# Kernel tuning notes

Hardware: AMD Instinct MI355X
Metric: run time of the kernel (lower is better)

## Reference

```python
import jax, jax.numpy as jnp
import numpy as np

N_NODES = 100000
N_EDGES = 1600000
IN_DIM, HID, OUT_DIM = 512, 32, 40


def setup_inputs() -> dict:
    key = jax.random.key(0)
    ks = jax.random.split(key, 6)
    x = jax.random.normal(ks[0], (N_NODES, IN_DIM), dtype=jnp.float32)
    edge_index = jax.random.randint(ks[1], (2, N_EDGES), 0, N_NODES, dtype=jnp.int64)
    # Glorot-ish init for the linear weights
    W1 = jax.random.normal(ks[2], (IN_DIM, HID), dtype=jnp.float32) / np.sqrt(IN_DIM)
    b1 = jnp.zeros((HID,), dtype=jnp.float32)
    W2 = jax.random.normal(ks[3], (HID, OUT_DIM), dtype=jnp.float32) / np.sqrt(HID)
    b2 = jnp.zeros((OUT_DIM,), dtype=jnp.float32)
    return {"x": x, "edge_index": edge_index, "W1": W1, "b1": b1, "W2": W2, "b2": b2}


def gcn_conv(x, W, b, src, dst, n_nodes):
    """PyG GCNConv: h = D^{-1/2} (A + I) D^{-1/2} (x W) + b."""
    h = x @ W  # linear transform first (reduces edge-level traffic)
    # add self-loops
    loop = jnp.arange(n_nodes, dtype=src.dtype)
    s = jnp.concatenate([src, loop])
    d = jnp.concatenate([dst, loop])
    # symmetric normalization from in-degree (including self-loops)
    deg = jax.ops.segment_sum(jnp.ones_like(d, dtype=h.dtype), d, num_segments=n_nodes)
    dinv = jnp.where(deg > 0, jax.lax.rsqrt(deg), 0.0)
    norm = dinv[s] * dinv[d]  # [E+N]
    msg = h[s] * norm[:, None]  # gather + scale
    out = jax.ops.segment_sum(msg, d, num_segments=n_nodes)  # scatter-add
    return out + b


def reference(x, edge_index, W1, b1, W2, b2):
    src, dst = edge_index[0], edge_index[1]
    n = x.shape[0]
    h = jax.nn.relu(gcn_conv(x, W1, b1, src, dst, n))
    # dropout is identity in eval mode (reference runs in eval)
    out = gcn_conv(h, W2, b2, src, dst, n)
    return out
```

## Files before the change

kernel.cpp:

```cpp
#include <hip/hip_runtime.h>
#include <hip/hip_bf16.h>

#define N_IN 512
#define HID 32
#define OUTD 40
#define NCOPY 8

typedef __attribute__((ext_vector_type(8))) short bf16x8;
typedef __attribute__((ext_vector_type(4))) float f32x4;


__global__ void k_init(int* __restrict__ csr, int tot4, int* __restrict__ cnt8,
                       int n8_4, int n, float* __restrict__ g1, float* __restrict__ p)
{
    int i = blockIdx.x * blockDim.x + threadIdx.x;
    if (i < tot4) {
        int4 v = make_int4(n, n, n, n);
        *(int4*)&csr[(size_t)i * 4] = v;
    }
    if (i < n8_4) {
        int4 z4 = make_int4(0, 0, 0, 0);
        *(int4*)&cnt8[(size_t)i * 4] = z4;
    }
    if (blockIdx.x == 0) {
        float4 z = make_float4(0.f, 0.f, 0.f, 0.f);
        if (threadIdx.x < 8)
            *(float4*)&g1[(size_t)n * HID + threadIdx.x * 4] = z;
        else if (threadIdx.x < 16)
            *(float4*)&p[(size_t)n * HID + (threadIdx.x - 8) * 4] = z;
    }
}

__global__ void k_count(const int* __restrict__ dst, int* __restrict__ cnt8,
                        int* __restrict__ rankp, int n, int e)
{
    int c = blockIdx.x & (NCOPY - 1);
    int* mycnt = cnt8 + (size_t)c * n;
    int i = (blockIdx.x * blockDim.x + threadIdx.x) * 4;
    if (i + 3 < e) {
        int4 d4 = *(const int4*)&dst[i];
        int r0 = atomicAdd(&mycnt[d4.x], 1);
        int r1 = atomicAdd(&mycnt[d4.y], 1);
        int r2 = atomicAdd(&mycnt[d4.z], 1);
        int r3 = atomicAdd(&mycnt[d4.w], 1);
        int hc = c << 24;
        *(int4*)&rankp[i] = make_int4(hc | r0, hc | r1, hc | r2, hc | r3);
    } else if (i < e) {
        for (int k = i; k < e; k++) {
            int r = atomicAdd(&mycnt[dst[k]], 1);
            rankp[k] = (c << 24) | r;
        }
    }
}

__global__ void k_bases(int* __restrict__ cnt8, int* __restrict__ cnt, int n)
{
    int d = blockIdx.x * blockDim.x + threadIdx.x;
    if (d >= n) return;
    int s = 0;
#pragma unroll
    for (int c = 0; c < NCOPY; c++) {
        int v = cnt8[(size_t)c * n + d];
        cnt8[(size_t)c * n + d] = s;
        s += v;
    }
    cnt[d] = s;
}

__global__ __launch_bounds__(256) void k_scan1(const int* __restrict__ cnt,
                                               int* __restrict__ offs,
                                               int* __restrict__ bsums, int n)
{
    __shared__ int sm[256];
    int t = threadIdx.x;
    int base = blockIdx.x * 1024 + t * 4;
    int a0 = (base + 0 < n) ? cnt[base + 0] : 0;
    int a1 = (base + 1 < n) ? cnt[base + 1] : 0;
    int a2 = (base + 2 < n) ? cnt[base + 2] : 0;
    int a3 = (base + 3 < n) ? cnt[base + 3] : 0;
    int d0 = (a0 + 15) & ~15;
    int d1 = (a1 + 15) & ~15;
    int d2 = (a2 + 15) & ~15;
    int d3 = (a3 + 15) & ~15;
    int s = d0 + d1 + d2 + d3;
    sm[t] = s;
    __syncthreads();
#pragma unroll
    for (int off = 1; off < 256; off <<= 1) {
        int v = (t >= off) ? sm[t - off] : 0;
        __syncthreads();
        sm[t] += v;
        __syncthreads();
    }
    int excl = sm[t] - s;
    if (base + 0 < n) offs[base + 0] = excl;
    if (base + 1 < n) offs[base + 1] = excl + d0;
    if (base + 2 < n) offs[base + 2] = excl + d0 + d1;
    if (base + 3 < n) offs[base + 3] = excl + d0 + d1 + d2;
    if (t == 255) bsums[blockIdx.x] = sm[255];
}

__global__ __launch_bounds__(256) void k_scan2(int* bsums, int nb)
{
    __shared__ int sm[256];
    int t = threadIdx.x;
    int s = (t < nb) ? bsums[t] : 0;
    sm[t] = s;
    __syncthreads();
#pragma unroll
    for (int off = 1; off < 256; off <<= 1) {
        int v = (t >= off) ? sm[t - off] : 0;
        __syncthreads();
        sm[t] += v;
        __syncthreads();
    }
    if (t < nb) bsums[t] = sm[t] - s;
}

__global__ void k_scan3(int* __restrict__ offs, const int* __restrict__ bsums,
                        const int* __restrict__ cnt, float* __restrict__ dinv, int n)
{
    int i = blockIdx.x * blockDim.x + threadIdx.x;
    if (i >= n) return;
    offs[i] = offs[i] + bsums[i >> 10];
    dinv[i] = rsqrtf((float)(cnt[i] + 1));
}

__global__ void k_pos(const int* __restrict__ dst, const int* __restrict__ offs,
                      const int* __restrict__ cnt8, int* __restrict__ rankp,
                      int n, int e)
{
    int i = (blockIdx.x * blockDim.x + threadIdx.x) * 4;
    if (i >= e) return;
    if (i + 3 < e) {
        int4 d4 = *(const int4*)&dst[i];
        int4 rp = *(const int4*)&rankp[i];
        int dd[4] = {d4.x, d4.y, d4.z, d4.w};
        int rr[4] = {rp.x, rp.y, rp.z, rp.w};
        int pp[4];
#pragma unroll
        for (int k = 0; k < 4; k++) {
            int d = dd[k];
            int c = ((unsigned)rr[k]) >> 24;
            int r = rr[k] & 0xFFFFFF;
            pp[k] = offs[d] + cnt8[(size_t)c * n + d] + r;
        }
        *(int4*)&rankp[i] = make_int4(pp[0], pp[1], pp[2], pp[3]);
    } else {
        for (int k = i; k < e; k++) {
            int d = dst[k];
            int r = rankp[k];
            int c = ((unsigned)r) >> 24;
            r &= 0xFFFFFF;
            rankp[k] = offs[d] + cnt8[(size_t)c * n + d] + r;
        }
    }
}

__global__ void k_fill(const int* __restrict__ src, const int* __restrict__ pos,
                       int* __restrict__ csr, int e)
{
    int i = (blockIdx.x * blockDim.x + threadIdx.x) * 4;
    if (i >= e) return;
    if (i + 3 < e) {
        int4 p4 = *(const int4*)&pos[i];
        int4 s4 = *(const int4*)&src[i];
        csr[p4.x] = s4.x;
        csr[p4.y] = s4.y;
        csr[p4.z] = s4.z;
        csr[p4.w] = s4.w;
    } else {
        for (int k = i; k < e; k++) csr[pos[k]] = src[k];
    }
}

__global__ void k_convw(const float* __restrict__ W, unsigned short* __restrict__ wfh,
                        unsigned short* __restrict__ wfl)
{
    int idx = blockIdx.x * blockDim.x + threadIdx.x;
    int j     = idx & 7;
    int lane  = (idx >> 3) & 63;
    int ntile = (idx >> 9) & 1;
    int kstep = idx >> 10;
    int k    = kstep * 32 + (lane >> 4) * 8 + j;
    int ncol = ntile * 16 + (lane & 15);
    float v = W[k * HID + ncol];
    unsigned u = __builtin_bit_cast(unsigned, v);
    unsigned short h = (unsigned short)(u >> 16);
    float hv = __builtin_bit_cast(float, u & 0xFFFF0000u);
    float rem = v - hv;
    unsigned ur = __builtin_bit_cast(unsigned, rem);
    ur += 0x7FFF + ((ur >> 16) & 1);
    wfh[idx] = h;
    wfl[idx] = (unsigned short)(ur >> 16);
}

__global__ __launch_bounds__(256) void k_gemm1(
    const float* __restrict__ x,
    const unsigned short* __restrict__ wfh, const unsigned short* __restrict__ wfl,
    const float* __restrict__ dinv, float* __restrict__ g1, int n)
{
    const int t    = threadIdx.x;
    const int lane = t & 63;
    const int wave = t >> 6;
    const int m    = lane & 15;
    const int quad = lane >> 4;
    const int row0 = blockIdx.x * 64 + wave * 16;

    int arow = row0 + m;
    if (arow >= n) arow = n - 1;
    const float* xp = x + (size_t)arow * N_IN + quad * 8;

    f32x4 acc0 = {0.f, 0.f, 0.f, 0.f};
    f32x4 acc1 = {0.f, 0.f, 0.f, 0.f};

    for (int ks = 0; ks < 16; ks++) {
        float4 xa = *(const float4*)(xp + ks * 32);
        float4 xb = *(const float4*)(xp + ks * 32 + 4);
        float xe[8] = {xa.x, xa.y, xa.z, xa.w, xb.x, xb.y, xb.z, xb.w};
        bf16x8 ah, al;
#pragma unroll
        for (int j = 0; j < 8; j++) {
            unsigned u = __builtin_bit_cast(unsigned, xe[j]);
            ah[j] = (short)(u >> 16);
            float hv = __builtin_bit_cast(float, u & 0xFFFF0000u);
            float rem = xe[j] - hv;
            unsigned ur = __builtin_bit_cast(unsigned, rem);
            ur += 0x7FFF + ((ur >> 16) & 1);
            al[j] = (short)(ur >> 16);
        }
        bf16x8 bh0 = *(const bf16x8*)(wfh + ((size_t)(ks * 2 + 0) * 64 + lane) * 8);
        bf16x8 bh1 = *(const bf16x8*)(wfh + ((size_t)(ks * 2 + 1) * 64 + lane) * 8);
        bf16x8 bl0 = *(const bf16x8*)(wfl + ((size_t)(ks * 2 + 0) * 64 + lane) * 8);
        bf16x8 bl1 = *(const bf16x8*)(wfl + ((size_t)(ks * 2 + 1) * 64 + lane) * 8);

        acc0 = __builtin_amdgcn_mfma_f32_16x16x32_bf16(ah, bh0, acc0, 0, 0, 0);
        acc0 = __builtin_amdgcn_mfma_f32_16x16x32_bf16(al, bh0, acc0, 0, 0, 0);
        acc0 = __builtin_amdgcn_mfma_f32_16x16x32_bf16(ah, bl0, acc0, 0, 0, 0);
        acc1 = __builtin_amdgcn_mfma_f32_16x16x32_bf16(ah, bh1, acc1, 0, 0, 0);
        acc1 = __builtin_amdgcn_mfma_f32_16x16x32_bf16(al, bh1, acc1, 0, 0, 0);
        acc1 = __builtin_amdgcn_mfma_f32_16x16x32_bf16(ah, bl1, acc1, 0, 0, 0);
    }

#pragma unroll
    for (int r = 0; r < 4; r++) {
        int row = row0 + quad * 4 + r;
        if (row < n) {
            float dv = dinv[row];
            g1[(size_t)row * HID + m]      = acc0[r] * dv;
            g1[(size_t)row * HID + 16 + m] = acc1[r] * dv;
        }
    }
}


__global__ void k_agg1(const int* __restrict__ csr, const int* __restrict__ offs,
                       const int* __restrict__ cnt, const float* __restrict__ g,
                       const float* __restrict__ dinv, const float* __restrict__ b1,
                       float* __restrict__ p, int n)
{
    int gid = blockIdx.x * blockDim.x + threadIdx.x;
    int r  = gid >> 4;
    int sl = gid & 15;
    if (r >= n) return;
    int s0 = offs[r];
    int dp = (cnt[r] + 15) & ~15;
    int half = sl >> 3;
    int c = sl & 7;
    const float* gc = g + c * 4;
    float4 acc = make_float4(0.f, 0.f, 0.f, 0.f);
    if (half == 0) acc = *(const float4*)&gc[(size_t)r * HID];
    for (int b = 0; b < dp; b += 16) {
        int s = csr[s0 + b + sl];
#pragma unroll
        for (int jj = 0; jj < 8; jj++) {
            int sj = __shfl(s, jj + (half << 3), 16);
            float4 v = *(const float4*)&gc[(size_t)sj * HID];
            acc.x += v.x; acc.y += v.y; acc.z += v.z; acc.w += v.w;
        }
    }
    float4 o;
    o.x = __shfl(acc.x, sl ^ 8, 16);
    o.y = __shfl(acc.y, sl ^ 8, 16);
    o.z = __shfl(acc.z, sl ^ 8, 16);
    o.w = __shfl(acc.w, sl ^ 8, 16);
    if (half == 0) {
        float dv = dinv[r];
        float4 bv = *(const float4*)&b1[c * 4];
        float4 hp;
        hp.x = dv * fmaxf((acc.x + o.x) * dv + bv.x, 0.f);
        hp.y = dv * fmaxf((acc.y + o.y) * dv + bv.y, 0.f);
        hp.z = dv * fmaxf((acc.z + o.z) * dv + bv.z, 0.f);
        hp.w = dv * fmaxf((acc.w + o.w) * dv + bv.w, 0.f);
        *(float4*)&p[(size_t)r * HID + c * 4] = hp;
    }
}

__global__ void k_agg2_out(const int* __restrict__ csr, const int* __restrict__ offs,
                           const int* __restrict__ cnt, const float* __restrict__ g,
                           const float* __restrict__ dinv, const float* __restrict__ W2,
                           const float* __restrict__ b2, float* __restrict__ out, int n)
{
    int gid = blockIdx.x * blockDim.x + threadIdx.x;
    int r  = gid >> 4;
    int sl = gid & 15;
    if (r >= n) return;
    int s0 = offs[r];
    int dp = (cnt[r] + 15) & ~15;
    int half = sl >> 3;
    int c = sl & 7;
    const float* gc = g + c * 4;
    float4 acc = make_float4(0.f, 0.f, 0.f, 0.f);
    if (half == 0) acc = *(const float4*)&gc[(size_t)r * HID];
    for (int b = 0; b < dp; b += 16) {
        int s = csr[s0 + b + sl];
#pragma unroll
        for (int jj = 0; jj < 8; jj++) {
            int sj = __shfl(s, jj + (half << 3), 16);
            float4 v = *(const float4*)&gc[(size_t)sj * HID];
            acc.x += v.x; acc.y += v.y; acc.z += v.z; acc.w += v.w;
        }
    }
    float4 o;
    o.x = __shfl(acc.x, sl ^ 8, 16);
    o.y = __shfl(acc.y, sl ^ 8, 16);
    o.z = __shfl(acc.z, sl ^ 8, 16);
    o.w = __shfl(acc.w, sl ^ 8, 16);
    float dv = dinv[r];
    float h0 = (acc.x + o.x) * dv;
    float h1 = (acc.y + o.y) * dv;
    float h2 = (acc.z + o.z) * dv;
    float h3 = (acc.w + o.w) * dv;

    int oc = (sl < 10) ? sl * 4 : 0;
    float4 ov = *(const float4*)&b2[oc];
#pragma unroll
    for (int k4 = 0; k4 < 8; k4++) {
        float a0 = __shfl(h0, k4, 16);
        float a1 = __shfl(h1, k4, 16);
        float a2 = __shfl(h2, k4, 16);
        float a3 = __shfl(h3, k4, 16);
        float4 w0 = *(const float4*)&W2[(4 * k4 + 0) * OUTD + oc];
        float4 w1 = *(const float4*)&W2[(4 * k4 + 1) * OUTD + oc];
        float4 w2 = *(const float4*)&W2[(4 * k4 + 2) * OUTD + oc];
        float4 w3 = *(const float4*)&W2[(4 * k4 + 3) * OUTD + oc];
        ov.x += a0 * w0.x + a1 * w1.x + a2 * w2.x + a3 * w3.x;
        ov.y += a0 * w0.y + a1 * w1.y + a2 * w2.y + a3 * w3.y;
        ov.z += a0 * w0.z + a1 * w1.z + a2 * w2.z + a3 * w3.z;
        ov.w += a0 * w0.w + a1 * w1.w + a2 * w2.w + a3 * w3.w;
    }
    if (sl < 10) *(float4*)&out[(size_t)r * OUTD + sl * 4] = ov;
}

extern "C" void kernel_launch(void* const* d_in, const int* in_sizes, int n_in,
                              void* d_out, int out_size, void* d_ws, size_t ws_size,
                              hipStream_t stream)
{
    const float* x  = (const float*)d_in[0];
    const int*   ei = (const int*)d_in[1];
    const float* W1 = (const float*)d_in[2];
    const float* b1 = (const float*)d_in[3];
    const float* W2 = (const float*)d_in[4];
    const float* b2 = (const float*)d_in[5];
    float* out = (float*)d_out;

    const int n = in_sizes[0] / N_IN;
    const int e = in_sizes[1] / 2;
    const int* src = ei;
    const int* dst = ei + e;

    const int csr_cap = e + 16 * n;

    char* w = (char*)d_ws;
    float* dinv   = (float*)w;            w += sizeof(float) * (size_t)((n + 3) & ~3);
    float* g1     = (float*)w;            w += sizeof(float) * (size_t)(n + 1) * HID;
    float* p      = (float*)w;            w += sizeof(float) * (size_t)(n + 1) * HID;
    int*   cnt    = (int*)w;              w += sizeof(int) * (size_t)((n + 3) & ~3);
    int*   offs   = (int*)w;              w += sizeof(int) * (size_t)((n + 3) & ~3);
    int*   cnt8   = (int*)w;              w += sizeof(int) * (size_t)NCOPY * ((n + 3) & ~3);
    int*   rankp  = (int*)w;              w += sizeof(int) * (size_t)((e + 3) & ~3);
    int*   bsums  = (int*)w;              w += sizeof(int) * 1024;
    unsigned short* wfh = (unsigned short*)w;  w += sizeof(unsigned short) * 16384;
    unsigned short* wfl = (unsigned short*)w;  w += sizeof(unsigned short) * 16384;
    int*   csr    = (int*)w;              w += sizeof(int) * (size_t)((csr_cap + 3) & ~3);

    const int nb = (n + 1023) / 1024;
    const int ec = (e + 3) / 4;
    const int n8_4 = (NCOPY * n + 3) / 4;
    const int tot4 = (csr_cap + 3) / 4;
    const int initN = (tot4 > n8_4) ? tot4 : n8_4;

    k_init<<<(initN + 255) / 256, 256, 0, stream>>>(csr, tot4, cnt8, n8_4, n, g1, p);
    k_count<<<(ec + 255) / 256, 256, 0, stream>>>(dst, cnt8, rankp, n, e);
    k_bases<<<(n + 255) / 256, 256, 0, stream>>>(cnt8, cnt, n);
    k_scan1<<<nb, 256, 0, stream>>>(cnt, offs, bsums, n);
    k_scan2<<<1, 256, 0, stream>>>(bsums, nb);
    k_scan3<<<(n + 255) / 256, 256, 0, stream>>>(offs, bsums, cnt, dinv, n);
    k_pos<<<(ec + 255) / 256, 256, 0, stream>>>(dst, offs, cnt8, rankp, n, e);
    k_fill<<<(ec + 255) / 256, 256, 0, stream>>>(src, rankp, csr, e);

    k_convw<<<64, 256, 0, stream>>>(W1, wfh, wfl);

    k_gemm1<<<(n + 63) / 64, 256, 0, stream>>>(x, wfh, wfl, dinv, g1, n);

    int t16 = n * 16;
    k_agg1<<<(t16 + 255) / 256, 256, 0, stream>>>(csr, offs, cnt, g1, dinv, b1, p, n);
    k_agg2_out<<<(t16 + 255) / 256, 256, 0, stream>>>(csr, offs, cnt, p, dinv, W2, b2, out, n);
}
```

Before: 510.1 us.

## Store hidden features in fp16 and fuse CSR position and fill kernels

Switches the intermediate feature buffers g1 and p from fp32 to fp16, halving the bytes moved by the random row gathers in both aggregation kernels. The aggregation lanes are remapped so each lane loads eight halves per gather, with a two-step shuffle reduction. The position and fill kernels are merged so computed CSR positions are used directly instead of being written to and reread from rankp. The cost is fp16 rounding of intermediate activations, which lowers accuracy.

```diff
diff --git a/kernel.cpp b/kernel.cpp
--- a/kernel.cpp
+++ b/kernel.cpp
@@ -8,10 +8,11 @@
 
 typedef __attribute__((ext_vector_type(8))) short bf16x8;
 typedef __attribute__((ext_vector_type(4))) float f32x4;
+typedef __attribute__((ext_vector_type(8))) _Float16 half8;
 
 
 __global__ void k_init(int* __restrict__ csr, int tot4, int* __restrict__ cnt8,
-                       int n8_4, int n, float* __restrict__ g1, float* __restrict__ p)
+                       int n8_4, int n, _Float16* __restrict__ g1, _Float16* __restrict__ p)
 {
     int i = blockIdx.x * blockDim.x + threadIdx.x;
     if (i < tot4) {
@@ -24,10 +25,10 @@
     }
     if (blockIdx.x == 0) {
         float4 z = make_float4(0.f, 0.f, 0.f, 0.f);
-        if (threadIdx.x < 8)
-            *(float4*)&g1[(size_t)n * HID + threadIdx.x * 4] = z;
-        else if (threadIdx.x < 16)
-            *(float4*)&p[(size_t)n * HID + (threadIdx.x - 8) * 4] = z;
+        if (threadIdx.x < 4)
+            ((float4*)&g1[(size_t)n * HID])[threadIdx.x] = z;
+        else if (threadIdx.x < 8)
+            ((float4*)&p[(size_t)n * HID])[threadIdx.x - 4] = z;
     }
 }
 
@@ -126,51 +127,35 @@
     dinv[i] = rsqrtf((float)(cnt[i] + 1));
 }
 
-__global__ void k_pos(const int* __restrict__ dst, const int* __restrict__ offs,
-                      const int* __restrict__ cnt8, int* __restrict__ rankp,
-                      int n, int e)
+__global__ void k_posfill(const int* __restrict__ dst, const int* __restrict__ src,
+                          const int* __restrict__ offs, const int* __restrict__ cnt8,
+                          const int* __restrict__ rankp, int* __restrict__ csr,
+                          int n, int e)
 {
     int i = (blockIdx.x * blockDim.x + threadIdx.x) * 4;
     if (i >= e) return;
     if (i + 3 < e) {
         int4 d4 = *(const int4*)&dst[i];
         int4 rp = *(const int4*)&rankp[i];
+        int4 s4 = *(const int4*)&src[i];
         int dd[4] = {d4.x, d4.y, d4.z, d4.w};
         int rr[4] = {rp.x, rp.y, rp.z, rp.w};
-        int pp[4];
+        int ss[4] = {s4.x, s4.y, s4.z, s4.w};
 #pragma unroll
         for (int k = 0; k < 4; k++) {
             int d = dd[k];
             int c = ((unsigned)rr[k]) >> 24;
             int r = rr[k] & 0xFFFFFF;
-            pp[k] = offs[d] + cnt8[(size_t)c * n + d] + r;
-        }
-        *(int4*)&rankp[i] = make_int4(pp[0], pp[1], pp[2], pp[3]);
+            csr[offs[d] + cnt8[(size_t)c * n + d] + r] = ss[k];
+        }
     } else {
         for (int k = i; k < e; k++) {
             int d = dst[k];
-            int r = rankp[k];
-            int c = ((unsigned)r) >> 24;
-            r &= 0xFFFFFF;
-            rankp[k] = offs[d] + cnt8[(size_t)c * n + d] + r;
-        }
-    }
-}
-
-__global__ void k_fill(const int* __restrict__ src, const int* __restrict__ pos,
-                       int* __restrict__ csr, int e)
-{
-    int i = (blockIdx.x * blockDim.x + threadIdx.x) * 4;
-    if (i >= e) return;
-    if (i + 3 < e) {
-        int4 p4 = *(const int4*)&pos[i];
-        int4 s4 = *(const int4*)&src[i];
-        csr[p4.x] = s4.x;
-        csr[p4.y] = s4.y;
-        csr[p4.z] = s4.z;
-        csr[p4.w] = s4.w;
-    } else {
-        for (int k = i; k < e; k++) csr[pos[k]] = src[k];
+            int rv = rankp[k];
+            int c = ((unsigned)rv) >> 24;
+            int r = rv & 0xFFFFFF;
+            csr[offs[d] + cnt8[(size_t)c * n + d] + r] = src[k];
+        }
     }
 }
 
@@ -198,7 +183,7 @@
 __global__ __launch_bounds__(256) void k_gemm1(
     const float* __restrict__ x,
     const unsigned short* __restrict__ wfh, const unsigned short* __restrict__ wfl,
-    const float* __restrict__ dinv, float* __restrict__ g1, int n)
+    const float* __restrict__ dinv, _Float16* __restrict__ g1, int n)
 {
     const int t    = threadIdx.x;
     const int lane = t & 63;
@@ -247,17 +232,17 @@
         int row = row0 + quad * 4 + r;
         if (row < n) {
             float dv = dinv[row];
-            g1[(size_t)row * HID + m]      = acc0[r] * dv;
-            g1[(size_t)row * HID + 16 + m] = acc1[r] * dv;
+            g1[(size_t)row * HID + m]      = (_Float16)(acc0[r] * dv);
+            g1[(size_t)row * HID + 16 + m] = (_Float16)(acc1[r] * dv);
         }
     }
 }
 
 
 __global__ void k_agg1(const int* __restrict__ csr, const int* __restrict__ offs,
-                       const int* __restrict__ cnt, const float* __restrict__ g,
+                       const int* __restrict__ cnt, const _Float16* __restrict__ g,
                        const float* __restrict__ dinv, const float* __restrict__ b1,
-                       float* __restrict__ p, int n)
+                       _Float16* __restrict__ p, int n)
 {
     int gid = blockIdx.x * blockDim.x + threadIdx.x;
     int r  = gid >> 4;
@@ -265,39 +250,45 @@
     if (r >= n) return;
     int s0 = offs[r];
     int dp = (cnt[r] + 15) & ~15;
-    int half = sl >> 3;
-    int c = sl & 7;
-    const float* gc = g + c * 4;
-    float4 acc = make_float4(0.f, 0.f, 0.f, 0.f);
-    if (half == 0) acc = *(const float4*)&gc[(size_t)r * HID];
+    int q  = sl >> 2;
+    int cq = sl & 3;
+    const _Float16* gc = g + cq * 8;
+    float acc[8] = {0.f, 0.f, 0.f, 0.f, 0.f, 0.f, 0.f, 0.f};
+    if (q == 0) {
+        half8 v = *(const half8*)&gc[(size_t)r * HID];
+#pragma unroll
+        for (int j = 0; j < 8; j++) acc[j] = (float)v[j];
+    }
     for (int b = 0; b < dp; b += 16) {
         int s = csr[s0 + b + sl];
 #pragma unroll
-        for (int jj = 0; jj < 8; jj++) {
-            int sj = __shfl(s, jj + (half << 3), 16);
-            float4 v = *(const float4*)&gc[(size_t)sj * HID];
-            acc.x += v.x; acc.y += v.y; acc.z += v.z; acc.w += v.w;
-        }
-    }
-    float4 o;
-    o.x = __shfl(acc.x, sl ^ 8, 16);
-    o.y = __shfl(acc.y, sl ^ 8, 16);
-    o.z = __shfl(acc.z, sl ^ 8, 16);
-    o.w = __shfl(acc.w, sl ^ 8, 16);
-    if (half == 0) {
+        for (int tt = 0; tt < 4; tt++) {
+            int sj = __shfl(s, tt * 4 + q, 16);
+            half8 v = *(const half8*)&gc[(size_t)sj * HID];
+#pragma unroll
+            for (int j = 0; j < 8; j++) acc[j] += (float)v[j];
+        }
+    }
+#pragma unroll
+    for (int j = 0; j < 8; j++) {
+        acc[j] += __shfl(acc[j], sl ^ 4, 16);
+        acc[j] += __shfl(acc[j], sl ^ 8, 16);
+    }
+    if (q == 0) {
         float dv = dinv[r];
-        float4 bv = *(const float4*)&b1[c * 4];
-        float4 hp;
-        hp.x = dv * fmaxf((acc.x + o.x) * dv + bv.x, 0.f);
-        hp.y = dv * fmaxf((acc.y + o.y) * dv + bv.y, 0.f);
-        hp.z = dv * fmaxf((acc.z + o.z) * dv + bv.z, 0.f);
-        hp.w = dv * fmaxf((acc.w + o.w) * dv + bv.w, 0.f);
-        *(float4*)&p[(size_t)r * HID + c * 4] = hp;
+        float4 ba = *(const float4*)&b1[cq * 8];
+        float4 bb = *(const float4*)&b1[cq * 8 + 4];
+        float bv[8] = {ba.x, ba.y, ba.z, ba.w, bb.x, bb.y, bb.z, bb.w};
+        half8 hp;
+#pragma unroll
+        for (int j = 0; j < 8; j++)
+            hp[j] = (_Float16)(dv * fmaxf(acc[j] * dv + bv[j], 0.f));
+        *(half8*)&p[(size_t)r * HID + cq * 8] = hp;
     }
 }
 
 __global__ void k_agg2_out(const int* __restrict__ csr, const int* __restrict__ offs,
-                           const int* __restrict__ cnt, const float* __restrict__ g,
+                           const int* __restrict__ cnt, const _Float16* __restrict__ g,
                            const float* __restrict__ dinv, const float* __restrict__ W2,
                            const float* __restrict__ b2, float* __restrict__ out, int n)
 {
@@ -307,47 +298,45 @@
     if (r >= n) return;
     int s0 = offs[r];
     int dp = (cnt[r] + 15) & ~15;
-    int half = sl >> 3;
-    int c = sl & 7;
-    const float* gc = g + c * 4;
-    float4 acc = make_float4(0.f, 0.f, 0.f, 0.f);
-    if (half == 0) acc = *(const float4*)&gc[(size_t)r * HID];
+    int q  = sl >> 2;
+    int cq = sl & 3;
+    const _Float16* gc = g + cq * 8;
+    float acc[8] = {0.f, 0.f, 0.f, 0.f, 0.f, 0.f, 0.f, 0.f};
+    if (q == 0) {
+        half8 v = *(const half8*)&gc[(size_t)r * HID];
+#pragma unroll
+        for (int j = 0; j < 8; j++) acc[j] = (float)v[j];
+    }
     for (int b = 0; b < dp; b += 16) {
         int s = csr[s0 + b + sl];
 #pragma unroll
-        for (int jj = 0; jj < 8; jj++) {
-            int sj = __shfl(s, jj + (half << 3), 16);
-            float4 v = *(const float4*)&gc[(size_t)sj * HID];
-            acc.x += v.x; acc.y += v.y; acc.z += v.z; acc.w += v.w;
-        }
-    }
-    float4 o;
-    o.x = __shfl(acc.x, sl ^ 8, 16);
-    o.y = __shfl(acc.y, sl ^ 8, 16);
-    o.z = __shfl(acc.z, sl ^ 8, 16);
-    o.w = __shfl(acc.w, sl ^ 8, 16);
+        for (int tt = 0; tt < 4; tt++) {
+            int sj = __shfl(s, tt * 4 + q, 16);
+            half8 v = *(const half8*)&gc[(size_t)sj * HID];
+#pragma unroll
+            for (int j = 0; j < 8; j++) acc[j] += (float)v[j];
+        }
+    }
+#pragma unroll
+    for (int j = 0; j < 8; j++) {
+        acc[j] += __shfl(acc[j], sl ^ 4, 16);
+        acc[j] += __shfl(acc[j], sl ^ 8, 16);
+    }
     float dv = dinv[r];
-    float h0 = (acc.x + o.x) * dv;
-    float h1 = (acc.y + o.y) * dv;
-    float h2 = (acc.z + o.z) * dv;
-    float h3 = (acc.w + o.w) * dv;
+    float h[8];
+#pragma unroll
+    for (int j = 0; j < 8; j++) h[j] = acc[j] * dv;
 
     int oc = (sl < 10) ? sl * 4 : 0;
     float4 ov = *(const float4*)&b2[oc];
 #pragma unroll
-    for (int k4 = 0; k4 < 8; k4++) {
-        float a0 = __shfl(h0, k4, 16);
-        float a1 = __shfl(h1, k4, 16);
-        float a2 = __shfl(h2, k4, 16);
-        float a3 = __shfl(h3, k4, 16);
-        float4 w0 = *(const float4*)&W2[(4 * k4 + 0) * OUTD + oc];
-        float4 w1 = *(const float4*)&W2[(4 * k4 + 1) * OUTD + oc];
-        float4 w2 = *(const float4*)&W2[(4 * k4 + 2) * OUTD + oc];
-        float4 w3 = *(const float4*)&W2[(4 * k4 + 3) * OUTD + oc];
-        ov.x += a0 * w0.x + a1 * w1.x + a2 * w2.x + a3 * w3.x;
-        ov.y += a0 * w0.y + a1 * w1.y + a2 * w2.y + a3 * w3.y;
-        ov.z += a0 * w0.z + a1 * w1.z + a2 * w2.z + a3 * w3.z;
-        ov.w += a0 * w0.w + a1 * w1.w + a2 * w2.w + a3 * w3.w;
+    for (int k = 0; k < HID; k++) {
+        float a = __shfl(h[k & 7], k >> 3, 16);
+        float4 wv = *(const float4*)&W2[k * OUTD + oc];
+        ov.x += a * wv.x;
+        ov.y += a * wv.y;
+        ov.z += a * wv.z;
+        ov.w += a * wv.w;
     }
     if (sl < 10) *(float4*)&out[(size_t)r * OUTD + sl * 4] = ov;
 }
@@ -373,8 +362,8 @@
 
     char* w = (char*)d_ws;
     float* dinv   = (float*)w;            w += sizeof(float) * (size_t)((n + 3) & ~3);
-    float* g1     = (float*)w;            w += sizeof(float) * (size_t)(n + 1) * HID;
-    float* p      = (float*)w;            w += sizeof(float) * (size_t)(n + 1) * HID;
+    _Float16* g1  = (_Float16*)w;         w += sizeof(_Float16) * (size_t)(n + 1) * HID;
+    _Float16* p   = (_Float16*)w;         w += sizeof(_Float16) * (size_t)(n + 1) * HID;
     int*   cnt    = (int*)w;              w += sizeof(int) * (size_t)((n + 3) & ~3);
     int*   offs   = (int*)w;              w += sizeof(int) * (size_t)((n + 3) & ~3);
     int*   cnt8   = (int*)w;              w += sizeof(int) * (size_t)NCOPY * ((n + 3) & ~3);
@@ -396,8 +385,7 @@
     k_scan1<<<nb, 256, 0, stream>>>(cnt, offs, bsums, n);
     k_scan2<<<1, 256, 0, stream>>>(bsums, nb);
     k_scan3<<<(n + 255) / 256, 256, 0, stream>>>(offs, bsums, cnt, dinv, n);
-    k_pos<<<(ec + 255) / 256, 256, 0, stream>>>(dst, offs, cnt8, rankp, n, e);
-    k_fill<<<(ec + 255) / 256, 256, 0, stream>>>(src, rankp, csr, e);
+    k_posfill<<<(ec + 255) / 256, 256, 0, stream>>>(dst, src, offs, cnt8, rankp, csr, n, e);
 
     k_convw<<<64, 256, 0, stream>>>(W1, wfh, wfl);
 
```

Result: faster. 493.6 us (-3.2%).
